# Performance work log

Measured on AMD Instinct MI355X. Metric: run time of the kernel, lower is better.

Reference implementation:

```python
import jax, jax.numpy as jnp
import numpy as np

N_ATOMS = 100000
N_MOLS = 2500
MAX_NB = 10
HID = 256
ATOM_FDIM = 151
FEAT_DIM = 200
FFN_HID = 1024
N_TASKS = 12
LN_EPS = 1e-5


def setup_inputs() -> dict:
    key = jax.random.key(0)
    ks = jax.random.split(key, 12)
    atoms_per_mol = N_ATOMS // N_MOLS  # 40
    starts = jnp.arange(N_MOLS, dtype=jnp.int32) * atoms_per_mol
    sizes = jnp.full((N_MOLS,), atoms_per_mol, dtype=jnp.int32)
    a_scope = jnp.stack([starts, sizes], axis=1)  # [M, 2]
    d_in = HID + ATOM_FDIM  # 407
    d_ff = 4 * HID          # 1024
    d_mol_in = HID + FEAT_DIM  # 456
    def lin(k, fan_in, shape):
        return jax.random.uniform(k, shape, jnp.float32, -1.0, 1.0) / np.sqrt(fan_in)
    return {
        "atom_output": jax.random.normal(ks[0], (N_ATOMS, HID), jnp.float32),
        "original_f_atoms": jax.random.uniform(ks[1], (N_ATOMS, ATOM_FDIM), jnp.float32),
        "a2a": jax.random.randint(ks[2], (N_ATOMS, MAX_NB), 0, N_ATOMS, jnp.int32),
        "a_scope": a_scope,
        "features_batch": jax.random.normal(ks[3], (N_MOLS, FEAT_DIM), jnp.float32),
        "W1": lin(ks[4], d_in, (d_in, d_ff)), "b1": jnp.zeros((d_ff,), jnp.float32),
        "W2": lin(ks[5], d_ff, (d_ff, HID)), "b2": jnp.zeros((HID,), jnp.float32),
        "ln_g": jnp.ones((HID,), jnp.float32), "ln_b": jnp.zeros((HID,), jnp.float32),
        "Wm1": lin(ks[6], d_mol_in, (d_mol_in, FFN_HID)), "bm1": jnp.zeros((FFN_HID,), jnp.float32),
        "Wm2": lin(ks[7], FFN_HID, (FFN_HID, N_TASKS)), "bm2": jnp.zeros((N_TASKS,), jnp.float32),
    }


def reference(atom_output, original_f_atoms, a2a, a_scope, features_batch,
              W1, b1, W2, b2, ln_g, ln_b, Wm1, bm1, Wm2, bm2):
    # select_neighbor_and_aggregate: gather neighbor embeddings and sum
    aggr = atom_output[a2a].sum(axis=1)                      # [N, HID]
    x = jnp.concatenate([original_f_atoms, aggr], axis=1)    # [N, HID+ATOM_FDIM]
    # PositionwiseFeedForward (dropout = identity at eval)
    h = jax.nn.relu(x @ W1 + b1) @ W2 + b2                   # [N, HID]
    # SublayerConnection with x=None: LayerNorm (dropout identity)
    mu = h.mean(axis=-1, keepdims=True)
    var = ((h - mu) ** 2).mean(axis=-1, keepdims=True)
    h = (h - mu) * jax.lax.rsqrt(var + LN_EPS) * ln_g + ln_b
    # Readout: mean over variable-length a_scope ranges (segment mean)
    starts = a_scope[:, 0]
    sizes = a_scope[:, 1]
    n_mols = a_scope.shape[0]
    seg_ids = jnp.searchsorted(starts, jnp.arange(h.shape[0], dtype=starts.dtype), side="right") - 1
    sums = jax.ops.segment_sum(h, seg_ids, num_segments=n_mols)   # [M, HID]
    mol = sums / sizes[:, None].astype(h.dtype)
    # concat molecule-level features, then mol FFN (2 layers)
    mol = jnp.concatenate([mol, features_batch], axis=1)          # [M, HID+FEAT_DIM]
    out = jax.nn.relu(mol @ Wm1 + bm1) @ Wm2 + bm2                # [M, N_TASKS]
    return out
```

## Files before the change

kernel.cpp:

```cpp
#include <hip/hip_runtime.h>

typedef __attribute__((ext_vector_type(8))) short bfrag;
typedef __attribute__((ext_vector_type(4))) float f32x4;

__device__ __forceinline__ float bf2f(unsigned short u) {
    union { unsigned u32; float f; } cv; cv.u32 = ((unsigned)u) << 16; return cv.f;
}
__device__ __forceinline__ unsigned short f2bf(float f) {
    union { float f; unsigned u; } cv; cv.f = f;
    unsigned u = cv.u;
    unsigned r = (u + 0x7fffu + ((u >> 16) & 1u)) >> 16;
    return (unsigned short)r;
}
__device__ __forceinline__ void gll16(const void* g, void* l) {
    __builtin_amdgcn_global_load_lds(
        (const __attribute__((address_space(1))) unsigned int*)g,
        (__attribute__((address_space(3))) unsigned int*)l, 16, 0, 0);
}

__global__ void to_bf16(const float* __restrict__ src, unsigned short* __restrict__ dst, size_t n) {
    size_t i = ((size_t)blockIdx.x * 256 + threadIdx.x) * 8;
    if (i >= n) return;
    float4 a = *reinterpret_cast<const float4*>(src + i);
    float4 b = *reinterpret_cast<const float4*>(src + i + 4);
    ushort4 o0 = {f2bf(a.x), f2bf(a.y), f2bf(a.z), f2bf(a.w)};
    ushort4 o1 = {f2bf(b.x), f2bf(b.y), f2bf(b.z), f2bf(b.w)};
    *reinterpret_cast<ushort4*>(dst + i) = o0;
    *reinterpret_cast<ushort4*>(dst + i + 4) = o1;
}

__global__ void transpose_pad(const float* __restrict__ W, unsigned short* __restrict__ WT,
                              int R, int Cn, int Kp, int split, int shiftA, int split2, int shiftB) {
    __shared__ unsigned short tile[32][33];
    int r0 = blockIdx.x * 32, c0 = blockIdx.y * 32;
#pragma unroll
    for (int j = 0; j < 4; j++) {
        int r = r0 + threadIdx.y + j * 8;
        int c = c0 + threadIdx.x;
        float v = (r < R) ? W[(size_t)r * Cn + c] : 0.f;
        tile[threadIdx.y + j * 8][threadIdx.x] = f2bf(v);
    }
    __syncthreads();
#pragma unroll
    for (int j = 0; j < 4; j++) {
        int c = c0 + threadIdx.y + j * 8;
        int r = r0 + threadIdx.x;
        int kn = (r < split) ? r + shiftA : (r < split2 ? r + shiftB : r);
        WT[(size_t)c * Kp + kn] = tile[threadIdx.x][threadIdx.y + j * 8];
    }
}

__global__ __launch_bounds__(256) void gather2(const unsigned short* __restrict__ abf,
                                               const float* __restrict__ f_atoms,
                                               const int* __restrict__ a2a,
                                               unsigned short* __restrict__ xb, int n_real) {
    int r = blockIdx.x * 4 + (threadIdx.x >> 6);
    int lane = threadIdx.x & 63;
    unsigned short* xrow = xb + (size_t)r * 448;
    if (r >= n_real) {
        *reinterpret_cast<ushort4*>(xrow + lane * 4) = ushort4{0, 0, 0, 0};
        if (lane < 48) *reinterpret_cast<ushort4*>(xrow + 256 + lane * 4) = ushort4{0, 0, 0, 0};
        return;
    }
    const int half = lane >> 5, lq = lane & 31;
    int v = (lane < 10) ? a2a[(size_t)r * 10 + lane] : 0;
    float acc[8] = {};
#pragma unroll
    for (int jj = 0; jj < 5; jj++) {
        int nbj = __shfl(v, jj * 2 + half);
        bfrag u = *reinterpret_cast<const bfrag*>(abf + (size_t)nbj * 256 + lq * 8);
#pragma unroll
        for (int k = 0; k < 8; k++) acc[k] += bf2f((unsigned short)u[k]);
    }
#pragma unroll
    for (int k = 0; k < 8; k++) acc[k] += __shfl_xor(acc[k], 32);
    if (half == 0) {
        bfrag o;
#pragma unroll
        for (int k = 0; k < 8; k++) o[k] = (short)f2bf(acc[k]);
        *reinterpret_cast<bfrag*>(xrow + lq * 8) = o;
    }
    const float* fr = f_atoms + (size_t)r * 151;
#pragma unroll
    for (int s = 0; s < 3; s++) {
        int c = lane + s * 64;
        if (c < 151) xrow[256 + c] = f2bf(fr[c]);
    }
    if (lane < 41) xrow[407 + lane] = 0;
}

template <int RELU>
__global__ __launch_bounds__(512, 2) void gemm256(const unsigned short* __restrict__ A,
                                                  const unsigned short* __restrict__ BT,
                                                  const float* __restrict__ bias,
                                                  unsigned short* __restrict__ C,
                                                  int NB, int N, int K) {
    __shared__ __align__(16) unsigned short As[256 * 64];
    __shared__ __align__(16) unsigned short Bs[128 * 64];
    const int t = threadIdx.x;
    const int lane = t & 63, wid = t >> 6;
    const int wm = wid >> 1, wn = wid & 1;
    const int la = lane & 15, hi = lane >> 4;

    const int nwg = gridDim.x, orig = blockIdx.x;
    const int q = nwg >> 3, r8 = nwg & 7;
    const int xcd = orig & 7, slot = orig >> 3;
    const int wgid = (xcd < r8 ? xcd * (q + 1) : r8 * (q + 1) + (xcd - r8) * q) + slot;
    const int bm = (wgid / NB) * 256, bn = (wgid % NB) * 128;

    f32x4 acc[4][4] = {};

    const int tr = t >> 3, ts = t & 7;
    const unsigned short* Ag = A + (size_t)(bm + tr) * K + (ts ^ (tr & 7)) * 8;
    const unsigned short* Bg = BT + (size_t)(bn + tr) * K + (ts ^ (tr & 7)) * 8;
    const int ldst = tr * 64 + ts * 8;

    for (int kt = 0; kt < K; kt += 64) {
        __builtin_amdgcn_s_barrier();
#pragma unroll
        for (int p = 0; p < 4; p++) gll16(Ag + (size_t)(p * 64) * K + kt, &As[p * 4096 + ldst]);
#pragma unroll
        for (int p = 0; p < 2; p++) gll16(Bg + (size_t)(p * 64) * K + kt, &Bs[p * 4096 + ldst]);
        asm volatile("s_waitcnt vmcnt(0)" ::: "memory");
        __builtin_amdgcn_s_barrier();
#pragma unroll
        for (int kk = 0; kk < 2; kk++) {
            bfrag a[4], b[4];
#pragma unroll
            for (int i = 0; i < 4; i++) {
                int row = wm * 64 + i * 16 + la;
                a[i] = *reinterpret_cast<const bfrag*>(&As[row * 64 + (((kk * 4 + hi) ^ (la & 7)) * 8)]);
            }
#pragma unroll
            for (int j = 0; j < 4; j++) {
                int row = wn * 64 + j * 16 + la;
                b[j] = *reinterpret_cast<const bfrag*>(&Bs[row * 64 + (((kk * 4 + hi) ^ (la & 7)) * 8)]);
            }
#pragma unroll
            for (int i = 0; i < 4; i++)
#pragma unroll
                for (int j = 0; j < 4; j++)
                    acc[i][j] = __builtin_amdgcn_mfma_f32_16x16x32_bf16(a[i], b[j], acc[i][j], 0, 0, 0);
        }
    }

#pragma unroll
    for (int j = 0; j < 4; j++) {
        int col = bn + wn * 64 + j * 16 + la;
        float bv = bias[col];
#pragma unroll
        for (int i = 0; i < 4; i++) {
            int rbase = bm + wm * 64 + i * 16 + hi * 4;
#pragma unroll
            for (int r = 0; r < 4; r++) {
                float v = acc[i][j][r] + bv;
                if (RELU) v = fmaxf(v, 0.f);
                C[(size_t)(rbase + r) * N + col] = f2bf(v);
            }
        }
    }
}

__global__ __launch_bounds__(512) void seg_ln_mean(const unsigned short* __restrict__ h,
                                                   const int* __restrict__ a_scope,
                                                   const float* __restrict__ g,
                                                   const float* __restrict__ b,
                                                   const float* __restrict__ feats,
                                                   unsigned short* __restrict__ mol, int n_mols) {
    __shared__ float part[8][256];
    int m = blockIdx.x, t = threadIdx.x;
    unsigned short* mrow = mol + (size_t)m * 512;
    if (m >= n_mols) {
        mrow[t] = 0;
        return;
    }
    int w = t >> 6, lane = t & 63;
    int start = a_scope[2 * m], size = a_scope[2 * m + 1];
    float4 gv = *reinterpret_cast<const float4*>(g + lane * 4);
    float4 bv = *reinterpret_cast<const float4*>(b + lane * 4);
    float a0 = 0.f, a1 = 0.f, a2 = 0.f, a3 = 0.f;
    for (int r = w; r < size; r += 8) {
        const unsigned short* hp = h + (size_t)(start + r) * 256 + lane * 4;
        ushort4 u = *reinterpret_cast<const ushort4*>(hp);
        float v0 = bf2f(u.x), v1 = bf2f(u.y), v2 = bf2f(u.z), v3 = bf2f(u.w);
        float s = v0 + v1 + v2 + v3;
        float q2 = v0 * v0 + v1 * v1 + v2 * v2 + v3 * v3;
#pragma unroll
        for (int off = 32; off; off >>= 1) {
            s += __shfl_xor(s, off);
            q2 += __shfl_xor(q2, off);
        }
        float mean = s * (1.f / 256.f);
        float var = q2 * (1.f / 256.f) - mean * mean;
        float rs = rsqrtf(var + 1e-5f);
        a0 += (v0 - mean) * rs * gv.x + bv.x;
        a1 += (v1 - mean) * rs * gv.y + bv.y;
        a2 += (v2 - mean) * rs * gv.z + bv.z;
        a3 += (v3 - mean) * rs * gv.w + bv.w;
    }
    part[w][lane * 4 + 0] = a0;
    part[w][lane * 4 + 1] = a1;
    part[w][lane * 4 + 2] = a2;
    part[w][lane * 4 + 3] = a3;
    __syncthreads();
    if (t < 256) {
        float sum = 0.f;
#pragma unroll
        for (int i = 0; i < 8; i++) sum += part[i][t];
        mrow[t] = f2bf(sum / (float)size);
    } else {
        int c = t - 256;
        float fv = (c < 200) ? feats[(size_t)m * 200 + c] : 0.f;
        mrow[256 + c] = f2bf(fv);
    }
}

__global__ void ffn2(const unsigned short* __restrict__ m1, const float* __restrict__ Wm2,
                     const float* __restrict__ bm2, float* __restrict__ out, int n_mols) {
    int wid = blockIdx.x * 4 + (threadIdx.x >> 6);
    if (wid >= n_mols) return;
    int lane = threadIdx.x & 63;
    float acc[12] = {};
    const unsigned short* row = m1 + (size_t)wid * 1024;
#pragma unroll 4
    for (int i = 0; i < 16; i++) {
        int k = i * 64 + lane;
        float v = bf2f(row[k]);
        const float* wr_ = Wm2 + (size_t)k * 12;
#pragma unroll
        for (int tsk = 0; tsk < 12; tsk++) acc[tsk] += v * wr_[tsk];
    }
#pragma unroll
    for (int tsk = 0; tsk < 12; tsk++) {
        float sv = acc[tsk];
#pragma unroll
        for (int off = 32; off; off >>= 1) sv += __shfl_xor(sv, off);
        if (lane == 0) out[(size_t)wid * 12 + tsk] = sv + bm2[tsk];
    }
}

extern "C" void kernel_launch(void* const* d_in, const int* in_sizes, int n_in,
                              void* d_out, int out_size, void* d_ws, size_t ws_size,
                              hipStream_t stream) {
    const float* atom_output = (const float*)d_in[0];
    const float* f_atoms     = (const float*)d_in[1];
    const int*   a2a         = (const int*)d_in[2];
    const int*   a_scope     = (const int*)d_in[3];
    const float* feats       = (const float*)d_in[4];
    const float* W1  = (const float*)d_in[5];
    const float* b1  = (const float*)d_in[6];
    const float* W2  = (const float*)d_in[7];
    const float* b2  = (const float*)d_in[8];
    const float* ln_g = (const float*)d_in[9];
    const float* ln_b = (const float*)d_in[10];
    const float* Wm1 = (const float*)d_in[11];
    const float* bm1 = (const float*)d_in[12];
    const float* Wm2 = (const float*)d_in[13];
    const float* bm2 = (const float*)d_in[14];
    float* out = (float*)d_out;

    char* ws = (char*)d_ws;
    size_t off = 0;
    auto alloc = [&](size_t bytes) {
        void* p = ws + off;
        off += (bytes + 255) & ~(size_t)255;
        return p;
    };
    unsigned short* h     = (unsigned short*)alloc((size_t)100096 * 256 * 2);
    unsigned short* h1    = (unsigned short*)alloc((size_t)100096 * 1024 * 2);
    unsigned short* xf    = (unsigned short*)alloc((size_t)100096 * 448 * 2);
    unsigned short* mol   = (unsigned short*)alloc((size_t)2560 * 512 * 2);
    unsigned short* m1b   = (unsigned short*)alloc((size_t)2560 * 1024 * 2);
    unsigned short* W1bT  = (unsigned short*)alloc((size_t)1024 * 448 * 2);
    unsigned short* W2bT  = (unsigned short*)alloc((size_t)256 * 1024 * 2);
    unsigned short* Wm1bT = (unsigned short*)alloc((size_t)1024 * 512 * 2);
    unsigned short* abf   = h1;

    transpose_pad<<<dim3(14, 32), dim3(32, 8), 0, stream>>>(W1, W1bT, 407, 1024, 448, 151, 256, 407, -151);
    transpose_pad<<<dim3(32, 8),  dim3(32, 8), 0, stream>>>(W2, W2bT, 1024, 256, 1024, 0, 0, 0, 0);
    transpose_pad<<<dim3(16, 32), dim3(32, 8), 0, stream>>>(Wm1, Wm1bT, 456, 1024, 512, 0, 0, 0, 0);

    to_bf16<<<12500, 256, 0, stream>>>(atom_output, abf, (size_t)100000 * 256);
    gather2<<<25024, 256, 0, stream>>>(abf, f_atoms, a2a, xf, 100000);

    gemm256<1><<<391 * 8, 512, 0, stream>>>(xf, W1bT, b1, h1, 8, 1024, 448);
    gemm256<0><<<391 * 2, 512, 0, stream>>>(h1, W2bT, b2, h, 2, 256, 1024);

    seg_ln_mean<<<2560, 512, 0, stream>>>(h, a_scope, ln_g, ln_b, feats, mol, 2500);
    gemm256<1><<<10 * 8, 512, 0, stream>>>(mol, Wm1bT, bm1, m1b, 8, 1024, 512);
    ffn2<<<625, 256, 0, stream>>>(m1b, Wm2, bm2, out, 2500);
}
```

Before: 392.3 us.

## Chunk the atom FFN into four passes so the hidden activations stay cache-resident

Splits the two atom-level FFN GEMMs into four row chunks that reuse one smaller intermediate buffer (about 25K rows instead of 100K). Each chunk's 1024-wide hidden activation is meant to stay in the large last-level cache between the W1 and W2 GEMMs, avoiding a full HBM round trip. The second GEMM now uses a new 128x128-tile, 256-thread kernel, giving more workgroups for the narrow N=256 output. The cost is more kernel launches and smaller grids per launch, which may leave CUs idle at chunk boundaries.

```diff
diff --git a/kernel.cpp b/kernel.cpp
--- a/kernel.cpp
+++ b/kernel.cpp
@@ -151,6 +151,78 @@
 #pragma unroll
         for (int i = 0; i < 4; i++) {
             int rbase = bm + wm * 64 + i * 16 + hi * 4;
+#pragma unroll
+            for (int r = 0; r < 4; r++) {
+                float v = acc[i][j][r] + bv;
+                if (RELU) v = fmaxf(v, 0.f);
+                C[(size_t)(rbase + r) * N + col] = f2bf(v);
+            }
+        }
+    }
+}
+
+template <int RELU>
+__global__ __launch_bounds__(256) void gemm97(const unsigned short* __restrict__ A,
+                                              const unsigned short* __restrict__ BT,
+                                              const float* __restrict__ bias,
+                                              unsigned short* __restrict__ C,
+                                              int NB, int N, int K) {
+    __shared__ __align__(16) unsigned short As[128 * 64];
+    __shared__ __align__(16) unsigned short Bs[128 * 64];
+    const int t = threadIdx.x;
+    const int lane = t & 63, w = t >> 6;
+    const int wr = w >> 1, wc = w & 1;
+    const int la = lane & 15, hi = lane >> 4;
+
+    const int nwg = gridDim.x, orig = blockIdx.x;
+    const int q = nwg >> 3, r8 = nwg & 7;
+    const int xcd = orig & 7, slot = orig >> 3;
+    const int wgid = (xcd < r8 ? xcd * (q + 1) : r8 * (q + 1) + (xcd - r8) * q) + slot;
+    const int bm = (wgid / NB) * 128, bn = (wgid % NB) * 128;
+
+    f32x4 acc[4][4] = {};
+
+    const int trow = t >> 3, tslot = t & 7;
+    const unsigned short* Ag = A + (size_t)(bm + trow) * K + (tslot ^ (trow & 7)) * 8;
+    const unsigned short* Bg = BT + (size_t)(bn + trow) * K + (tslot ^ (trow & 7)) * 8;
+    const int ldst = trow * 64 + tslot * 8;
+
+    for (int kt = 0; kt < K; kt += 64) {
+        __builtin_amdgcn_s_barrier();
+#pragma unroll
+        for (int p = 0; p < 4; p++) gll16(Ag + (size_t)(p * 32) * K + kt, &As[p * 2048 + ldst]);
+#pragma unroll
+        for (int p = 0; p < 4; p++) gll16(Bg + (size_t)(p * 32) * K + kt, &Bs[p * 2048 + ldst]);
+        asm volatile("s_waitcnt vmcnt(0)" ::: "memory");
+        __builtin_amdgcn_s_barrier();
+#pragma unroll
+        for (int kk = 0; kk < 2; kk++) {
+            bfrag a[4], b[4];
+#pragma unroll
+            for (int i = 0; i < 4; i++) {
+                int row = wr * 64 + i * 16 + la;
+                a[i] = *reinterpret_cast<const bfrag*>(&As[row * 64 + (((kk * 4 + hi) ^ (la & 7)) * 8)]);
+            }
+#pragma unroll
+            for (int j = 0; j < 4; j++) {
+                int row = wc * 64 + j * 16 + la;
+                b[j] = *reinterpret_cast<const bfrag*>(&Bs[row * 64 + (((kk * 4 + hi) ^ (la & 7)) * 8)]);
+            }
+#pragma unroll
+            for (int i = 0; i < 4; i++)
+#pragma unroll
+                for (int j = 0; j < 4; j++)
+                    acc[i][j] = __builtin_amdgcn_mfma_f32_16x16x32_bf16(a[i], b[j], acc[i][j], 0, 0, 0);
+        }
+    }
+
+#pragma unroll
+    for (int j = 0; j < 4; j++) {
+        int col = bn + wc * 64 + j * 16 + la;
+        float bv = bias[col];
+#pragma unroll
+        for (int i = 0; i < 4; i++) {
+            int rbase = bm + wr * 64 + i * 16 + hi * 4;
 #pragma unroll
             for (int r = 0; r < 4; r++) {
                 float v = acc[i][j][r] + bv;
@@ -267,14 +339,14 @@
         return p;
     };
     unsigned short* h     = (unsigned short*)alloc((size_t)100096 * 256 * 2);
-    unsigned short* h1    = (unsigned short*)alloc((size_t)100096 * 1024 * 2);
+    unsigned short* h1c   = (unsigned short*)alloc((size_t)25088 * 1024 * 2);
     unsigned short* xf    = (unsigned short*)alloc((size_t)100096 * 448 * 2);
     unsigned short* mol   = (unsigned short*)alloc((size_t)2560 * 512 * 2);
     unsigned short* m1b   = (unsigned short*)alloc((size_t)2560 * 1024 * 2);
     unsigned short* W1bT  = (unsigned short*)alloc((size_t)1024 * 448 * 2);
     unsigned short* W2bT  = (unsigned short*)alloc((size_t)256 * 1024 * 2);
     unsigned short* Wm1bT = (unsigned short*)alloc((size_t)1024 * 512 * 2);
-    unsigned short* abf   = h1;
+    unsigned short* abf   = h;
 
     transpose_pad<<<dim3(14, 32), dim3(32, 8), 0, stream>>>(W1, W1bT, 407, 1024, 448, 151, 256, 407, -151);
     transpose_pad<<<dim3(32, 8),  dim3(32, 8), 0, stream>>>(W2, W2bT, 1024, 256, 1024, 0, 0, 0, 0);
@@ -283,8 +355,14 @@
     to_bf16<<<12500, 256, 0, stream>>>(atom_output, abf, (size_t)100000 * 256);
     gather2<<<25024, 256, 0, stream>>>(abf, f_atoms, a2a, xf, 100000);
 
-    gemm256<1><<<391 * 8, 512, 0, stream>>>(xf, W1bT, b1, h1, 8, 1024, 448);
-    gemm256<0><<<391 * 2, 512, 0, stream>>>(h1, W2bT, b2, h, 2, 256, 1024);
+    const int cnt[4] = {98, 98, 98, 97};
+    int row0 = 0;
+    for (int c = 0; c < 4; c++) {
+        int mrows = cnt[c] * 256;
+        gemm256<1><<<cnt[c] * 8, 512, 0, stream>>>(xf + (size_t)row0 * 448, W1bT, b1, h1c, 8, 1024, 448);
+        gemm97<0><<<(mrows / 128) * 2, 256, 0, stream>>>(h1c, W2bT, b2, h + (size_t)row0 * 256, 2, 256, 1024);
+        row0 += mrows;
+    }
 
     seg_ln_mean<<<2560, 512, 0, stream>>>(h, a_scope, ln_g, ln_b, feats, mol, 2500);
     gemm256<1><<<10 * 8, 512, 0, stream>>>(mol, Wm1bT, bm1, m1b, 8, 1024, 512);
```

Result: slower. 418.0 us (+6.6%).
